# Kernel optimization log

Measured on AMD Instinct MI355X. Metric: run time of the kernel, lower is better.

Reference implementation:

```python
import jax, jax.numpy as jnp
import numpy as np

B, T, C, H = 2, 2048, 1024, 16
HS = C // H  # head_size = 64
EPS = 1e-5


def _layernorm(x, w, b):
    mu = jnp.mean(x, axis=-1, keepdims=True)
    var = jnp.mean(jnp.square(x - mu), axis=-1, keepdims=True)
    return (x - mu) * jax.lax.rsqrt(var + EPS) * w + b


def setup_inputs() -> dict:
    key = jax.random.key(0)
    ks = jax.random.split(key, 12)
    s_attn = 1.0 / np.sqrt(C)
    s_ff1 = 1.0 / np.sqrt(C)
    s_ff2 = 1.0 / np.sqrt(4 * C)
    return {
        "x": jax.random.normal(ks[0], (B, T, C), dtype=jnp.float32),
        "ln1_w": jnp.ones((C,), jnp.float32),
        "ln1_b": jnp.zeros((C,), jnp.float32),
        "Wq": jax.random.normal(ks[1], (H, C, HS), jnp.float32) * s_attn,
        "Wk": jax.random.normal(ks[2], (H, C, HS), jnp.float32) * s_attn,
        "Wv": jax.random.normal(ks[3], (H, C, HS), jnp.float32) * s_attn,
        "proj_w": jax.random.normal(ks[4], (C, C), jnp.float32) * s_attn,
        "proj_b": jnp.zeros((C,), jnp.float32),
        "ln2_w": jnp.ones((C,), jnp.float32),
        "ln2_b": jnp.zeros((C,), jnp.float32),
        "fc1_w": jax.random.normal(ks[5], (C, 4 * C), jnp.float32) * s_ff1,
        "fc1_b": jnp.zeros((4 * C,), jnp.float32),
        "fc2_w": jax.random.normal(ks[6], (4 * C, C), jnp.float32) * s_ff2,
        "fc2_b": jnp.zeros((C,), jnp.float32),
    }


def reference(x, ln1_w, ln1_b, Wq, Wk, Wv, proj_w, proj_b, ln2_w, ln2_b, fc1_w, fc1_b, fc2_w, fc2_b):
    Bx, Tx, Cx = x.shape
    # --- self-attention with pre-norm residual ---
    h = _layernorm(x, ln1_w, ln1_b)                       # [B,T,C]
    q = jnp.einsum("btc,hcd->bhtd", h, Wq)                 # [B,H,T,HS]
    k = jnp.einsum("btc,hcd->bhtd", h, Wk)
    v = jnp.einsum("btc,hcd->bhtd", h, Wv)
    # NOTE: original code applies NO 1/sqrt(d) scaling -- keep faithful.
    wei = jnp.einsum("bhtd,bhsd->bhts", q, k)              # [B,H,T,T]
    causal = jnp.tril(jnp.ones((Tx, Tx), dtype=bool))
    wei = jnp.where(causal, wei, -jnp.inf)
    wei = jax.nn.softmax(wei, axis=-1)
    attn = jnp.einsum("bhts,bhsd->bhtd", wei, v)           # [B,H,T,HS]
    attn = attn.transpose(0, 2, 1, 3).reshape(Bx, Tx, Cx)  # concat heads
    sa = attn @ proj_w + proj_b                            # output projection
    x = x + sa
    # --- FFN with pre-norm residual ---
    h2 = _layernorm(x, ln2_w, ln2_b)
    ff = jax.nn.relu(h2 @ fc1_w + fc1_b) @ fc2_w + fc2_b
    return x + ff
```

## Files before the change

### kernel.cpp

```cpp
#include <hip/hip_runtime.h>
#include <hip/hip_bf16.h>

#define Bn 2
#define Tn 2048
#define Cn 1024
#define Hn 16
#define HSn 64
#define Mn (Bn*Tn)
#define LN_EPS 1e-5f

typedef unsigned short u16;
typedef __attribute__((ext_vector_type(8))) short bf16x8;
typedef __attribute__((ext_vector_type(4))) float f32x4;

#define MFMA16(a,b,c) __builtin_amdgcn_mfma_f32_16x16x32_bf16(a, b, c, 0, 0, 0)
#define GLL16(g,l) __builtin_amdgcn_global_load_lds( \
    (const __attribute__((address_space(1))) void*)(g), \
    (__attribute__((address_space(3))) void*)(l), 16, 0, 0)

__device__ __forceinline__ u16 f2b(float f) {
    unsigned int u = __float_as_uint(f);
    unsigned int r = (u + 0x7FFFu + ((u >> 16) & 1u)) >> 16;
    return (u16)r;
}
__device__ __forceinline__ float b2f(unsigned u) {
    return __uint_as_float(u << 16);
}
__device__ __forceinline__ unsigned cvtpk(float lo, float hi) {
    unsigned r;
    asm("v_cvt_pk_bf16_f32 %0, %1, %2" : "=v"(r) : "v"(lo), "v"(hi));
    return r;
}

__device__ __forceinline__ void trans_tile(
    const float* __restrict__ in, u16* __restrict__ out,
    int R, int C, int r0, int c0c, float (*t)[68], int tid)
{
#pragma unroll
    for (int it = 0; it < 4; it++) {
        int r = it * 16 + (tid >> 4);
        *(float4*)&t[r][(tid & 15) * 4] =
            *(const float4*)(in + (size_t)(r0 + r) * C + c0c + (tid & 15) * 4);
    }
    __syncthreads();
    int c = tid >> 2, seg = tid & 3;
    union { u16 u[8]; uint4 q; } pk;
#pragma unroll
    for (int hq = 0; hq < 2; hq++) {
#pragma unroll
        for (int j = 0; j < 8; j++) pk.u[j] = f2b(t[seg * 16 + hq * 8 + j][c]);
        *(uint4*)(out + (size_t)(c0c + c) * R + r0 + seg * 16 + hq * 8) = pk.q;
    }
}

__global__ __launch_bounds__(256) void repack_all(
    const float* __restrict__ Wq, const float* __restrict__ Wk,
    const float* __restrict__ Wv, u16* __restrict__ WtQKV,
    const float* __restrict__ projw, u16* __restrict__ WtP,
    const float* __restrict__ fc1w, u16* __restrict__ Wt1,
    const float* __restrict__ fc2w, u16* __restrict__ Wt2)
{
    __shared__ float t[64][68];
    const int bid = (int)blockIdx.x, tid = threadIdx.x;
    if (bid < 768) {
        int z = bid >> 8, rem = bid & 255, h = rem >> 4, c0 = (rem & 15) * 64;
        const float* in = (z == 0 ? Wq : z == 1 ? Wk : Wv) + (size_t)h * 65536;
        u16* outb = WtQKV + (size_t)(z * 1024 + h * 64) * 1024;
        trans_tile(in, outb, 1024, 64, c0, 0, t, tid);
    } else if (bid < 1024) {
        int idx = bid - 768, bx = idx & 15, by = idx >> 4;
        trans_tile(projw, WtP, 1024, 1024, by * 64, bx * 64, t, tid);
    } else if (bid < 2048) {
        int idx = bid - 1024, bx = idx & 63, by = idx >> 6;
        trans_tile(fc1w, Wt1, 1024, 4096, by * 64, bx * 64, t, tid);
    } else {
        int idx = bid - 2048, bx = idx & 15, by = idx >> 4;
        trans_tile(fc2w, Wt2, 4096, 1024, by * 64, bx * 64, t, tid);
    }
}

__global__ __launch_bounds__(256) void ln_bf16(
    const float* __restrict__ x, const float* __restrict__ w,
    const float* __restrict__ bvec, u16* __restrict__ out)
{
    int row  = blockIdx.x * 4 + (threadIdx.x >> 6);
    int lane = threadIdx.x & 63;
    const float* xr = x + (size_t)row * Cn;
    float4 v[4];
    float s = 0.f, sq = 0.f;
#pragma unroll
    for (int i = 0; i < 4; i++) {
        v[i] = *(const float4*)(xr + lane * 4 + i * 256);
        s  += v[i].x + v[i].y + v[i].z + v[i].w;
        sq += v[i].x * v[i].x + v[i].y * v[i].y + v[i].z * v[i].z + v[i].w * v[i].w;
    }
#pragma unroll
    for (int off = 1; off < 64; off <<= 1) {
        s  += __shfl_xor(s, off);
        sq += __shfl_xor(sq, off);
    }
    float mu   = s * (1.f / Cn);
    float var  = sq * (1.f / Cn) - mu * mu;
    float rstd = rsqrtf(var + LN_EPS);
    u16* orow = out + (size_t)row * Cn;
#pragma unroll
    for (int i = 0; i < 4; i++) {
        float4 w4 = *(const float4*)(w    + lane * 4 + i * 256);
        float4 b4 = *(const float4*)(bvec + lane * 4 + i * 256);
        union { u16 u[4]; uint2 q; } pk;
        pk.u[0] = f2b((v[i].x - mu) * rstd * w4.x + b4.x);
        pk.u[1] = f2b((v[i].y - mu) * rstd * w4.y + b4.y);
        pk.u[2] = f2b((v[i].z - mu) * rstd * w4.z + b4.z);
        pk.u[3] = f2b((v[i].w - mu) * rstd * w4.w + b4.w);
        *(uint2*)(orow + lane * 4 + i * 256) = pk.q;
    }
}

__global__ __launch_bounds__(256) void ln_bf16_b(
    const u16* __restrict__ x, const float* __restrict__ w,
    const float* __restrict__ bvec, u16* __restrict__ out)
{
    int row  = blockIdx.x * 4 + (threadIdx.x >> 6);
    int lane = threadIdx.x & 63;
    const u16* xr = x + (size_t)row * Cn + lane * 16;
    float v[16];
    float s = 0.f, sq = 0.f;
#pragma unroll
    for (int i = 0; i < 2; i++) {
        uint4 q = *(const uint4*)(xr + i * 8);
        float* vv = v + i * 8;
        vv[0] = b2f(q.x & 0xffffu); vv[1] = b2f(q.x >> 16);
        vv[2] = b2f(q.y & 0xffffu); vv[3] = b2f(q.y >> 16);
        vv[4] = b2f(q.z & 0xffffu); vv[5] = b2f(q.z >> 16);
        vv[6] = b2f(q.w & 0xffffu); vv[7] = b2f(q.w >> 16);
    }
#pragma unroll
    for (int j = 0; j < 16; j++) { s += v[j]; sq += v[j] * v[j]; }
#pragma unroll
    for (int off = 1; off < 64; off <<= 1) {
        s  += __shfl_xor(s, off);
        sq += __shfl_xor(sq, off);
    }
    float mu   = s * (1.f / Cn);
    float var  = sq * (1.f / Cn) - mu * mu;
    float rstd = rsqrtf(var + LN_EPS);
    u16* orow = out + (size_t)row * Cn + lane * 16;
#pragma unroll
    for (int i = 0; i < 2; i++) {
        union { u16 u[8]; uint4 q; } pk;
#pragma unroll
        for (int j = 0; j < 8; j++) {
            int col = lane * 16 + i * 8 + j;
            pk.u[j] = f2b((v[i * 8 + j] - mu) * rstd * w[col] + bvec[col]);
        }
        *(uint4*)(orow + i * 8) = pk.q;
    }
}

template<int OBF, int BIAS, int RELU>
__global__ __launch_bounds__(512, 2) void gemm_8ph(
    const u16* __restrict__ A, const u16* __restrict__ Bt,
    const float* __restrict__ bias, void* Cout,
    int M, int N, int K, int NT)
{
    __shared__ u16 lds[65536];
    const int tid = threadIdx.x, l = tid & 63, w = tid >> 6;
    const int wm = w >> 2, wn = w & 3;
    const int g = l >> 4, c16 = l & 15;

    const int nwg = (int)gridDim.x, cpx = nwg >> 3;
    const int bid = (int)blockIdx.x;
    const int sbid = (bid & 7) * cpx + (bid >> 3);
    const int m0 = (sbid / NT) * 256, n0 = (sbid % NT) * 256;

    const int sr = tid >> 3;
    const int ss = ((tid & 7) ^ (sr & 7)) << 3;
    const u16* Asrc = A  + (size_t)(m0 + sr) * K + ss;
    const u16* Bsrc = Bt + (size_t)(n0 + sr) * K + ss;
    const int dst0 = tid * 8;

#define ST_A8(d_, h_, kt_) do {                                              \
        GLL16(Asrc + (size_t)((h_) * 128) * K + (size_t)(kt_) * 64,          \
              &lds[(d_) * 32768 + (h_) * 8192 + dst0]);                      \
        GLL16(Asrc + (size_t)((h_) * 128 + 64) * K + (size_t)(kt_) * 64,     \
              &lds[(d_) * 32768 + (h_) * 8192 + 4096 + dst0]);               \
    } while (0)
#define ST_B8(d_, h_, kt_) do {                                              \
        GLL16(Bsrc + (size_t)((h_) * 128) * K + (size_t)(kt_) * 64,          \
              &lds[(d_) * 32768 + 16384 + (h_) * 8192 + dst0]);              \
        GLL16(Bsrc + (size_t)((h_) * 128 + 64) * K + (size_t)(kt_) * 64,     \
              &lds[(d_) * 32768 + 16384 + (h_) * 8192 + 4096 + dst0]);       \
    } while (0)
#define LDA8(d_, mi_, s_) (*(const bf16x8*)&lds[(d_) * 32768 +               \
        (wm * 128 + (mi_) * 16 + c16) * 64 +                                  \
        ((((s_) * 4 + g) ^ ((wm * 128 + (mi_) * 16 + c16) & 7)) << 3)])
#define LDB8(d_, nj_, s_) (*(const bf16x8*)&lds[(d_) * 32768 + 16384 +       \
        (wn * 64 + (nj_) * 16 + c16) * 64 +                                   \
        ((((s_) * 4 + g) ^ ((wn * 64 + (nj_) * 16 + c16) & 7)) << 3)])
#define PH_HEAD() do {                                                       \
        __builtin_amdgcn_s_barrier();                                        \
        asm volatile("s_waitcnt lgkmcnt(0)" ::: "memory");                   \
        __builtin_amdgcn_sched_barrier(0);                                   \
        __builtin_amdgcn_s_setprio(1);                                       \
    } while (0)
#define PH_MFMA(NH_) do {                                                    \
        _Pragma("unroll")                                                    \
        for (int mi = 0; mi < 8; mi++) {                                     \
            acc[mi][2*(NH_)]   = MFMA16(aF[mi], bF[0], acc[mi][2*(NH_)]);    \
            acc[mi][2*(NH_)+1] = MFMA16(aF[mi], bF[1], acc[mi][2*(NH_)+1]);  \
        }                                                                    \
    } while (0)

    f32x4 acc[8][4];
#pragma unroll
    for (int i = 0; i < 8; i++)
#pragma unroll
        for (int j = 0; j < 4; j++) acc[i][j] = (f32x4){0.f, 0.f, 0.f, 0.f};

    const int nk = K >> 6;
    ST_A8(0, 0, 0); ST_A8(0, 1, 0); ST_B8(0, 0, 0); ST_B8(0, 1, 0);
    ST_A8(1, 0, 1); ST_A8(1, 1, 1);
    asm volatile("s_waitcnt vmcnt(4)" ::: "memory");
    __builtin_amdgcn_s_barrier();

    bf16x8 aF[8], bF[2];
    for (int m = 0; m < nk; m++) {
        const int d = m & 1, dn = d ^ 1;
#pragma unroll
        for (int mi = 0; mi < 8; mi++) aF[mi] = LDA8(d, mi, 0);
        bF[0] = LDB8(d, 0, 0); bF[1] = LDB8(d, 1, 0);
        if (m + 1 < nk) ST_B8(dn, 0, m + 1);
        PH_HEAD(); PH_MFMA(0);
        __builtin_amdgcn_s_setprio(0);
        __builtin_amdgcn_s_barrier();
        bF[0] = LDB8(d, 2, 0); bF[1] = LDB8(d, 3, 0);
        if (m + 1 < nk) ST_B8(dn, 1, m + 1);
        PH_HEAD(); PH_MFMA(1);
        __builtin_amdgcn_s_setprio(0);
        __builtin_amdgcn_s_barrier();
#pragma unroll
        for (int mi = 0; mi < 8; mi++) aF[mi] = LDA8(d, mi, 1);
        bF[0] = LDB8(d, 0, 1); bF[1] = LDB8(d, 1, 1);
        PH_HEAD(); PH_MFMA(0);
        __builtin_amdgcn_s_setprio(0);
        __builtin_amdgcn_s_barrier();
        bF[0] = LDB8(d, 2, 1); bF[1] = LDB8(d, 3, 1);
        if (m + 2 < nk) { ST_A8(d, 0, m + 2); ST_A8(d, 1, m + 2); }
        PH_HEAD(); PH_MFMA(1);
        __builtin_amdgcn_s_setprio(0);
        if (m + 1 < nk) {
            if (m + 2 < nk) asm volatile("s_waitcnt vmcnt(4)" ::: "memory");
            else            asm volatile("s_waitcnt vmcnt(0)" ::: "memory");
        }
        __builtin_amdgcn_s_barrier();
    }
#undef ST_A8
#undef ST_B8
#undef LDA8
#undef LDB8
#undef PH_HEAD
#undef PH_MFMA

#pragma unroll
    for (int mi = 0; mi < 8; mi++)
#pragma unroll
        for (int nj = 0; nj < 4; nj++) {
            const int coln = n0 + wn * 64 + nj * 16 + c16;
            float bv = BIAS ? bias[coln] : 0.f;
#pragma unroll
            for (int reg = 0; reg < 4; reg++) {
                int rowm = m0 + wm * 128 + mi * 16 + 4 * g + reg;
                float v = acc[mi][nj][reg] + bv;
                if (RELU) v = fmaxf(v, 0.f);
                if (OBF) ((u16*)Cout)[(size_t)rowm * N + coln] = f2b(v);
                else     ((float*)Cout)[(size_t)rowm * N + coln] = v;
            }
        }
}

__global__ __launch_bounds__(512, 1) void gemm_qkv(
    const u16* __restrict__ A, const u16* __restrict__ Bt,
    u16* __restrict__ Cout)
{
    __shared__ u16 lds[57344];
    const int tid = threadIdx.x, l = tid & 63, w = tid >> 6;
    const int wm = w >> 1, wn = w & 1;
    const int g = l >> 4, c16 = l & 15;
    const int K = 1024, N = 3072;

    const int bid = (int)blockIdx.x;
    const int sbid = (bid & 7) * 32 + (bid >> 3);
    const int m0 = (sbid >> 4) * 256, n0 = (sbid & 15) * 192;

    const int sr = tid >> 3;
    const int ss = ((tid & 7) ^ (sr & 7)) << 3;
    const u16* Asrc = A  + (size_t)(m0 + sr) * K + ss;
    const u16* Bsrc = Bt + (size_t)(n0 + sr) * K + ss;
    const int dst0 = tid * 8;

#define ST_A(d_, h_, kt_) do {                                               \
        GLL16(Asrc + (size_t)((h_) * 128) * K + (size_t)(kt_) * 64,          \
              &lds[(d_) * 16384 + (h_) * 8192 + dst0]);                      \
        GLL16(Asrc + (size_t)((h_) * 128 + 64) * K + (size_t)(kt_) * 64,     \
              &lds[(d_) * 16384 + (h_) * 8192 + 4096 + dst0]);               \
    } while (0)
#define ST_B1(d_, seg_, kt_)                                                 \
        GLL16(Bsrc + (size_t)((seg_) * 64) * K + (size_t)(kt_) * 64,         \
              &lds[32768 + (d_) * 12288 + (seg_) * 4096 + dst0])
#define LDA(d_, mi_, s_) (*(const bf16x8*)&lds[(d_) * 16384 +                \
        (wm * 64 + (mi_) * 16 + c16) * 64 +                                   \
        ((((s_) * 4 + g) ^ ((wm * 64 + (mi_) * 16 + c16) & 7)) << 3)])
#define LDB(d_, nj_, s_) (*(const bf16x8*)&lds[32768 + (d_) * 12288 +        \
        (wn * 96 + (nj_) * 16 + c16) * 64 +                                   \
        ((((s_) * 4 + g) ^ ((wn * 96 + (nj_) * 16 + c16) & 7)) << 3)])
#define PH_HEAD() do {                                                       \
        __builtin_amdgcn_s_barrier();                                        \
        asm volatile("s_waitcnt lgkmcnt(0)" ::: "memory");                   \
        __builtin_amdgcn_sched_barrier(0);                                   \
        __builtin_amdgcn_s_setprio(1);                                       \
    } while (0)
#define PH_MFMA(NH_) do {                                                    \
        _Pragma("unroll")                                                    \
        for (int mi = 0; mi < 4; mi++) {                                     \
            acc[mi][3*(NH_)]   = MFMA16(aF[mi], bF[0], acc[mi][3*(NH_)]);    \
            acc[mi][3*(NH_)+1] = MFMA16(aF[mi], bF[1], acc[mi][3*(NH_)+1]);  \
            acc[mi][3*(NH_)+2] = MFMA16(aF[mi], bF[2], acc[mi][3*(NH_)+2]);  \
        }                                                                    \
    } while (0)

    f32x4 acc[4][6];
#pragma unroll
    for (int i = 0; i < 4; i++)
#pragma unroll
        for (int j = 0; j < 6; j++) acc[i][j] = (f32x4){0.f, 0.f, 0.f, 0.f};

    const int nk = 16;
    ST_A(0, 0, 0); ST_A(0, 1, 0);
    ST_B1(0, 0, 0); ST_B1(0, 1, 0); ST_B1(0, 2, 0);
    ST_A(1, 0, 1); ST_A(1, 1, 1);
    asm volatile("s_waitcnt vmcnt(4)" ::: "memory");
    __builtin_amdgcn_s_barrier();

    bf16x8 aF[4], bF[3];
    for (int m = 0; m < nk; m++) {
        const int d = m & 1, dn = d ^ 1;
#pragma unroll
        for (int mi = 0; mi < 4; mi++) aF[mi] = LDA(d, mi, 0);
        bF[0] = LDB(d, 0, 0); bF[1] = LDB(d, 1, 0); bF[2] = LDB(d, 2, 0);
        if (m + 1 < nk) { ST_B1(dn, 0, m + 1); ST_B1(dn, 1, m + 1); }
        PH_HEAD(); PH_MFMA(0);
        __builtin_amdgcn_s_setprio(0);
        __builtin_amdgcn_s_barrier();
        bF[0] = LDB(d, 3, 0); bF[1] = LDB(d, 4, 0); bF[2] = LDB(d, 5, 0);
        if (m + 1 < nk) ST_B1(dn, 2, m + 1);
        PH_HEAD(); PH_MFMA(1);
        __builtin_amdgcn_s_setprio(0);
        __builtin_amdgcn_s_barrier();
#pragma unroll
        for (int mi = 0; mi < 4; mi++) aF[mi] = LDA(d, mi, 1);
        bF[0] = LDB(d, 0, 1); bF[1] = LDB(d, 1, 1); bF[2] = LDB(d, 2, 1);
        PH_HEAD(); PH_MFMA(0);
        __builtin_amdgcn_s_setprio(0);
        __builtin_amdgcn_s_barrier();
        bF[0] = LDB(d, 3, 1); bF[1] = LDB(d, 4, 1); bF[2] = LDB(d, 5, 1);
        if (m + 2 < nk) { ST_A(d, 0, m + 2); ST_A(d, 1, m + 2); }
        PH_HEAD(); PH_MFMA(1);
        __builtin_amdgcn_s_setprio(0);
        if (m + 1 < nk) {
            if (m + 2 < nk) asm volatile("s_waitcnt vmcnt(4)" ::: "memory");
            else            asm volatile("s_waitcnt vmcnt(0)" ::: "memory");
        }
        __builtin_amdgcn_s_barrier();
    }
#undef ST_A
#undef ST_B1
#undef LDA
#undef LDB
#undef PH_HEAD
#undef PH_MFMA

#pragma unroll
    for (int mi = 0; mi < 4; mi++)
#pragma unroll
        for (int nj = 0; nj < 6; nj++) {
            const int coln = n0 + wn * 96 + nj * 16 + c16;
#pragma unroll
            for (int reg = 0; reg < 4; reg++) {
                int rowm = m0 + wm * 64 + mi * 16 + 4 * g + reg;
                Cout[(size_t)rowm * N + coln] = f2b(acc[mi][nj][reg]);
            }
        }
}

__global__ __launch_bounds__(512, 2) void gemm_fc2(
    const u16* __restrict__ A, const u16* __restrict__ Bt,
    u16* __restrict__ part)
{
    __shared__ u16 lds[65536];
    const int tid = threadIdx.x, l = tid & 63, w = tid >> 6;
    const int wm = w >> 2, wn = w & 3;
    const int g = l >> 4, c16 = l & 15;

    const int bid = (int)blockIdx.x;
    const int sbid = (bid & 7) * 32 + (bid >> 3);
    const int chunk = sbid >> 6, t = sbid & 63;
    const int m0 = (t >> 2) * 256, n0 = (t & 3) * 256;
    const int kB = chunk << 10;

    const int sr = tid >> 3;
    const int ss = ((tid & 7) ^ (sr & 7)) << 3;
    const u16* Asrc = A  + (size_t)(m0 + sr) * 4096 + kB + ss;
    const u16* Bsrc = Bt + (size_t)(n0 + sr) * 4096 + kB + ss;
    const int dst0 = tid * 8;

#define ST_A8(d_, h_, kt_) do {                                              \
        GLL16(Asrc + (size_t)((h_) * 128) * 4096 + (size_t)(kt_) * 64,       \
              &lds[(d_) * 32768 + (h_) * 8192 + dst0]);                      \
        GLL16(Asrc + (size_t)((h_) * 128 + 64) * 4096 + (size_t)(kt_) * 64,  \
              &lds[(d_) * 32768 + (h_) * 8192 + 4096 + dst0]);               \
    } while (0)
#define ST_B8(d_, h_, kt_) do {                                              \
        GLL16(Bsrc + (size_t)((h_) * 128) * 4096 + (size_t)(kt_) * 64,       \
              &lds[(d_) * 32768 + 16384 + (h_) * 8192 + dst0]);              \
        GLL16(Bsrc + (size_t)((h_) * 128 + 64) * 4096 + (size_t)(kt_) * 64,  \
              &lds[(d_) * 32768 + 16384 + (h_) * 8192 + 4096 + dst0]);       \
    } while (0)
#define LDA8(d_, mi_, s_) (*(const bf16x8*)&lds[(d_) * 32768 +               \
        (wm * 128 + (mi_) * 16 + c16) * 64 +                                  \
        ((((s_) * 4 + g) ^ ((wm * 128 + (mi_) * 16 + c16) & 7)) << 3)])
#define LDB8(d_, nj_, s_) (*(const bf16x8*)&lds[(d_) * 32768 + 16384 +       \
        (wn * 64 + (nj_) * 16 + c16) * 64 +                                   \
        ((((s_) * 4 + g) ^ ((wn * 64 + (nj_) * 16 + c16) & 7)) << 3)])
#define PH_HEAD() do {                                                       \
        __builtin_amdgcn_s_barrier();                                        \
        asm volatile("s_waitcnt lgkmcnt(0)" ::: "memory");                   \
        __builtin_amdgcn_sched_barrier(0);                                   \
        __builtin_amdgcn_s_setprio(1);                                       \
    } while (0)
#define PH_MFMA(NH_) do {                                                    \
        _Pragma("unroll")                                                    \
        for (int mi = 0; mi < 8; mi++) {                                     \
            acc[mi][2*(NH_)]   = MFMA16(aF[mi], bF[0], acc[mi][2*(NH_)]);    \
            acc[mi][2*(NH_)+1] = MFMA16(aF[mi], bF[1], acc[mi][2*(NH_)+1]);  \
        }                                                                    \
    } while (0)

    f32x4 acc[8][4];
#pragma unroll
    for (int i = 0; i < 8; i++)
#pragma unroll
        for (int j = 0; j < 4; j++) acc[i][j] = (f32x4){0.f, 0.f, 0.f, 0.f};

    const int nk = 16;
    ST_A8(0, 0, 0); ST_A8(0, 1, 0); ST_B8(0, 0, 0); ST_B8(0, 1, 0);
    ST_A8(1, 0, 1); ST_A8(1, 1, 1);
    asm volatile("s_waitcnt vmcnt(4)" ::: "memory");
    __builtin_amdgcn_s_barrier();

    bf16x8 aF[8], bF[2];
    for (int m = 0; m < nk; m++) {
        const int d = m & 1, dn = d ^ 1;
#pragma unroll
        for (int mi = 0; mi < 8; mi++) aF[mi] = LDA8(d, mi, 0);
        bF[0] = LDB8(d, 0, 0); bF[1] = LDB8(d, 1, 0);
        if (m + 1 < nk) ST_B8(dn, 0, m + 1);
        PH_HEAD(); PH_MFMA(0);
        __builtin_amdgcn_s_setprio(0);
        __builtin_amdgcn_s_barrier();
        bF[0] = LDB8(d, 2, 0); bF[1] = LDB8(d, 3, 0);
        if (m + 1 < nk) ST_B8(dn, 1, m + 1);
        PH_HEAD(); PH_MFMA(1);
        __builtin_amdgcn_s_setprio(0);
        __builtin_amdgcn_s_barrier();
#pragma unroll
        for (int mi = 0; mi < 8; mi++) aF[mi] = LDA8(d, mi, 1);
        bF[0] = LDB8(d, 0, 1); bF[1] = LDB8(d, 1, 1);
        PH_HEAD(); PH_MFMA(0);
        __builtin_amdgcn_s_setprio(0);
        __builtin_amdgcn_s_barrier();
        bF[0] = LDB8(d, 2, 1); bF[1] = LDB8(d, 3, 1);
        if (m + 2 < nk) { ST_A8(d, 0, m + 2); ST_A8(d, 1, m + 2); }
        PH_HEAD(); PH_MFMA(1);
        __builtin_amdgcn_s_setprio(0);
        if (m + 1 < nk) {
            if (m + 2 < nk) asm volatile("s_waitcnt vmcnt(4)" ::: "memory");
            else            asm volatile("s_waitcnt vmcnt(0)" ::: "memory");
        }
        __builtin_amdgcn_s_barrier();
    }
#undef ST_A8
#undef ST_B8
#undef LDA8
#undef LDB8
#undef PH_HEAD
#undef PH_MFMA

    u16* pp = part + (size_t)chunk * 4194304;
#pragma unroll
    for (int mi = 0; mi < 8; mi++)
#pragma unroll
        for (int nj = 0; nj < 4; nj++) {
            const int coln = n0 + wn * 64 + nj * 16 + c16;
#pragma unroll
            for (int reg = 0; reg < 4; reg++) {
                int rowm = m0 + wm * 128 + mi * 16 + 4 * g + reg;
                pp[(size_t)rowm * 1024 + coln] = f2b(acc[mi][nj][reg]);
            }
        }
}

__global__ __launch_bounds__(256) void splitk_reduce(
    const u16* __restrict__ part, const u16* __restrict__ x1,
    const float* __restrict__ bias, float* __restrict__ out)
{
    size_t i = ((size_t)blockIdx.x * 256 + threadIdx.x) * 4;
    int col = (int)(i & 1023);
    float4 bv = *(const float4*)(bias + col);
    uint2 xv = *(const uint2*)(x1 + i);
    float s0 = b2f(xv.x & 0xffffu) + bv.x;
    float s1 = b2f(xv.x >> 16)     + bv.y;
    float s2 = b2f(xv.y & 0xffffu) + bv.z;
    float s3 = b2f(xv.y >> 16)     + bv.w;
#pragma unroll
    for (int c = 0; c < 4; c++) {
        uint2 p = *(const uint2*)(part + (size_t)c * 4194304 + i);
        s0 += b2f(p.x & 0xffffu);
        s1 += b2f(p.x >> 16);
        s2 += b2f(p.y & 0xffffu);
        s3 += b2f(p.y >> 16);
    }
    float4 r; r.x = s0; r.y = s1; r.z = s2; r.w = s3;
    *(float4*)(out + i) = r;
}

template<int OBF, int BIAS, int RES, int RELU>
__global__ __launch_bounds__(256) void gemm_n64(
    const u16* __restrict__ A, const u16* __restrict__ Bt,
    const float* __restrict__ bias, const float* res,
    void* Cout, int M, int N, int K)
{
    __shared__ u16 As[2][8192];
    __shared__ u16 Bs[2][4096];
    const int tid = threadIdx.x;
    const int l = tid & 63, w = tid >> 6;
    const int wr = w >> 1, wc = w & 1;
    const int g = l >> 4, c16 = l & 15;
    const int m0 = blockIdx.y * 128, n0 = blockIdx.x * 64;

    const u16* a_src[4];
    int a_dst[4];
#pragma unroll
    for (int i = 0; i < 4; i++) {
        int G = tid + 256 * i, r = G >> 3, sl = G & 7;
        a_src[i] = A + (size_t)(m0 + r) * K + ((sl ^ (r & 7)) << 3);
        a_dst[i] = G * 8;
    }
    const u16* b_src[2];
    int b_dst[2];
#pragma unroll
    for (int i = 0; i < 2; i++) {
        int G = tid + 256 * i, r = G >> 3, sl = G & 7;
        b_src[i] = Bt + (size_t)(n0 + r) * K + ((sl ^ (r & 7)) << 3);
        b_dst[i] = G * 8;
    }

    f32x4 acc[4][2];
#pragma unroll
    for (int i = 0; i < 4; i++)
#pragma unroll
        for (int j = 0; j < 2; j++) acc[i][j] = (f32x4){0.f, 0.f, 0.f, 0.f};

#define STAGE_N64(nb, k0) do {                                   \
        GLL16(a_src[0] + (k0), &As[nb][a_dst[0]]);               \
        GLL16(a_src[1] + (k0), &As[nb][a_dst[1]]);               \
        GLL16(a_src[2] + (k0), &As[nb][a_dst[2]]);               \
        GLL16(a_src[3] + (k0), &As[nb][a_dst[3]]);               \
        GLL16(b_src[0] + (k0), &Bs[nb][b_dst[0]]);               \
        GLL16(b_src[1] + (k0), &Bs[nb][b_dst[1]]);               \
    } while (0)

    STAGE_N64(0, 0);
    __syncthreads();

    int cur = 0;
    for (int k0 = 0; k0 < K; k0 += 64) {
        if (k0 + 64 < K) STAGE_N64(cur ^ 1, k0 + 64);
        const u16* AsC = As[cur];
        const u16* BsC = Bs[cur];
        bf16x8 af[4][2], bfr[2][2];
#pragma unroll
        for (int fi = 0; fi < 4; fi++) {
            int r = wr * 64 + fi * 16 + c16;
            af[fi][0] = *(const bf16x8*)&AsC[r * 64 + (((g    ) ^ (r & 7)) << 3)];
            af[fi][1] = *(const bf16x8*)&AsC[r * 64 + (((4 + g) ^ (r & 7)) << 3)];
        }
#pragma unroll
        for (int fj = 0; fj < 2; fj++) {
            int r = wc * 32 + fj * 16 + c16;
            bfr[fj][0] = *(const bf16x8*)&BsC[r * 64 + (((g    ) ^ (r & 7)) << 3)];
            bfr[fj][1] = *(const bf16x8*)&BsC[r * 64 + (((4 + g) ^ (r & 7)) << 3)];
        }
#pragma unroll
        for (int fi = 0; fi < 4; fi++)
#pragma unroll
            for (int fj = 0; fj < 2; fj++) {
                acc[fi][fj] = MFMA16(af[fi][0], bfr[fj][0], acc[fi][fj]);
                acc[fi][fj] = MFMA16(af[fi][1], bfr[fj][1], acc[fi][fj]);
            }
        __syncthreads();
        cur ^= 1;
    }
#undef STAGE_N64

#pragma unroll
    for (int fi = 0; fi < 4; fi++)
#pragma unroll
        for (int fj = 0; fj < 2; fj++) {
            int coln = n0 + wc * 32 + fj * 16 + c16;
            float bv = BIAS ? bias[coln] : 0.f;
#pragma unroll
            for (int reg = 0; reg < 4; reg++) {
                int rowm = m0 + wr * 64 + fi * 16 + 4 * g + reg;
                float v = acc[fi][fj][reg] + bv;
                if (RES) v += res[(size_t)rowm * N + coln];
                if (RELU) v = fmaxf(v, 0.f);
                if (OBF) ((u16*)Cout)[(size_t)rowm * N + coln] = f2b(v);
                else     ((float*)Cout)[(size_t)rowm * N + coln] = v;
            }
        }
}

__global__ __launch_bounds__(256) void v_transpose(
    const u16* __restrict__ qkv, u16* __restrict__ vT)
{
    int t0 = blockIdx.x * 64, h = blockIdx.y, b = blockIdx.z;
    __shared__ u16 t[64][72];
    int tid = threadIdx.x;
#pragma unroll
    for (int it = 0; it < 2; it++) {
        int r = it * 32 + (tid >> 3);
        int cs = (tid & 7) * 8;
        *(uint4*)&t[r][cs] =
            *(const uint4*)(qkv + (size_t)(b * 2048 + t0 + r) * 3072 + 2048 + h * 64 + cs);
    }
    __syncthreads();
    int d = tid >> 2, seg = tid & 3;
    union { u16 u[8]; uint4 q; } pk;
#pragma unroll
    for (int hq = 0; hq < 2; hq++) {
#pragma unroll
        for (int j = 0; j < 8; j++) pk.u[j] = t[seg * 16 + hq * 8 + j][d];
        *(uint4*)(vT + (size_t)((b * 16 + h) * 64 + d) * 2048 + t0 + seg * 16 + hq * 8) = pk.q;
    }
}

__global__ __launch_bounds__(512) void attn_mfma(
    const u16* __restrict__ qkv, const u16* __restrict__ vT,
    u16* __restrict__ outb)
{
    __shared__ u16 smem[24576];
    u16* KsB = smem;
    u16* VsB = smem + 8192;
    u16* PsB = smem + 16384;
    const int tid = threadIdx.x, l = tid & 63, w = tid >> 6;
    const int g = l >> 4, c16 = l & 15;
    const int qg = w & 3, kg = w >> 2;
    const int kg32 = kg * 32, kg64 = kg * 64;
    const int bh = blockIdx.y, b = bh >> 4, h = bh & 15;
    const int bx = (int)blockIdx.x;
    const int qt = (bh < 16) ? (15 - bx) : bx;
    const int r0 = qt * 128;
    const int wq0 = r0 + qg * 32;

    bf16x8 qf[2][2];
#pragma unroll
    for (int grp = 0; grp < 2; grp++) {
        const u16* qrow = qkv + (size_t)(b * 2048 + wq0 + grp * 16 + c16) * 3072 + h * 64;
        qf[grp][0] = *(const bf16x8*)(qrow + g * 8);
        qf[grp][1] = *(const bf16x8*)(qrow + 32 + g * 8);
    }

    const int kr = tid >> 3, ks = (tid & 7) ^ (kr & 7);
    const u16* kgp = qkv + (size_t)(b * 2048) * 3072 + 1024 + h * 64;
    const u16* vgp = vT + (size_t)((b * 16 + h) * 64) * 2048;

    float lrow[2] = {0.f, 0.f};
    f32x4 oacc[2][4];
#pragma unroll
    for (int grp = 0; grp < 2; grp++)
#pragma unroll
        for (int i = 0; i < 4; i++) oacc[grp][i] = (f32x4){0.f, 0.f, 0.f, 0.f};

    const int prow0 = (qg * 32 + c16) * 128;
    const int swz   = (c16 & 7) << 4;

#define STAGE_KV(nb, s0) do {                                                  \
        GLL16(kgp + (size_t)((s0) + kr) * 3072 + ks * 8, &KsB[(nb)*4096 + tid*8]); \
        GLL16(vgp + (size_t)kr * 2048 + (s0) + ks * 8, &VsB[(nb)*4096 + tid*8]);   \
    } while (0)

    STAGE_KV(0, 0);
    asm volatile("s_waitcnt vmcnt(0)" ::: "memory");
    __builtin_amdgcn_sched_barrier(0);
    __builtin_amdgcn_s_barrier();

    const int nt = 2 * qt + 2;
    int cur = 0;
    for (int kt = 0; kt < nt; kt++) {
        if (kt + 1 < nt) STAGE_KV(cur ^ 1, (kt + 1) * 64);
        if (kt > 0) {
            if (kt + 1 < nt) asm volatile("s_waitcnt vmcnt(2)" ::: "memory");
            else             asm volatile("s_waitcnt vmcnt(0)" ::: "memory");
            __builtin_amdgcn_sched_barrier(0);
            __builtin_amdgcn_s_barrier();
        }
        const u16* KsC = &KsB[cur * 4096];
        const u16* VsC = &VsB[cur * 4096];
        const int s0 = kt * 64;

        bf16x8 kf0[2], kf1[2];
#pragma unroll
        for (int fj = 0; fj < 2; fj++) {
            int r = kg32 + fj * 16 + c16;
            kf0[fj] = *(const bf16x8*)&KsC[r * 64 + ((g       ^ (r & 7)) << 3)];
            kf1[fj] = *(const bf16x8*)&KsC[r * 64 + (((4 + g) ^ (r & 7)) << 3)];
        }
#pragma unroll
        for (int grp = 0; grp < 2; grp++) {
            f32x4 sc[2];
            sc[0] = (f32x4){0.f, 0.f, 0.f, 0.f};
            sc[1] = (f32x4){0.f, 0.f, 0.f, 0.f};
#pragma unroll
            for (int fj = 0; fj < 2; fj++) {
                sc[fj] = MFMA16(kf0[fj], qf[grp][0], sc[fj]);
                sc[fj] = MFMA16(kf1[fj], qf[grp][1], sc[fj]);
            }
            const int qgl = wq0 + grp * 16 + c16;
            if (s0 + kg32 + 31 > wq0 + grp * 16) {
#pragma unroll
                for (int fj = 0; fj < 2; fj++)
#pragma unroll
                    for (int reg = 0; reg < 4; reg++)
                        if (s0 + kg32 + fj * 16 + 4 * g + reg > qgl)
                            sc[fj][reg] = -1e30f;
            }
#pragma unroll
            for (int fj = 0; fj < 2; fj++) {
                float p0 = __expf(sc[fj][0]);
                float p1 = __expf(sc[fj][1]);
                float p2 = __expf(sc[fj][2]);
                float p3 = __expf(sc[fj][3]);
                lrow[grp] += (p0 + p1) + (p2 + p3);
                uint2 pk;
                pk.x = cvtpk(p0, p1);
                pk.y = cvtpk(p2, p3);
                *(uint2*)((char*)PsB + prow0 + grp * 2048 +
                          ((kg64 + fj * 32 + 8 * g) ^ swz)) = pk;
            }
        }
        bf16x8 pa0 = *(const bf16x8*)((const char*)PsB + prow0 +
                                      ((kg64 + 16 * g) ^ swz));
        bf16x8 pa1 = *(const bf16x8*)((const char*)PsB + prow0 + 2048 +
                                      ((kg64 + 16 * g) ^ swz));
#pragma unroll
        for (int fd = 0; fd < 4; fd++) {
            int r = fd * 16 + c16;
            bf16x8 vf = *(const bf16x8*)&VsC[r * 64 + (((4 * kg + g) ^ (r & 7)) << 3)];
            oacc[0][fd] = MFMA16(pa0, vf, oacc[0][fd]);
            oacc[1][fd] = MFMA16(pa1, vf, oacc[1][fd]);
        }
        __builtin_amdgcn_s_barrier();
        cur ^= 1;
    }
#undef STAGE_KV

#pragma unroll
    for (int grp = 0; grp < 2; grp++) {
        lrow[grp] += __shfl_xor(lrow[grp], 16);
        lrow[grp] += __shfl_xor(lrow[grp], 32);
    }

    __syncthreads();
    float* scr = (float*)smem;
    const int sbase = qg * 2304 + l * 36;
    if (kg == 1) {
#pragma unroll
        for (int grp = 0; grp < 2; grp++) {
#pragma unroll
            for (int fd = 0; fd < 4; fd++)
                *(f32x4*)&scr[sbase + grp * 16 + fd * 4] = oacc[grp][fd];
            scr[sbase + 32 + grp] = lrow[grp];
        }
    }
    __syncthreads();
    if (kg == 0) {
#pragma unroll
        for (int grp = 0; grp < 2; grp++) {
#pragma unroll
            for (int fd = 0; fd < 4; fd++)
                oacc[grp][fd] += *(const f32x4*)&scr[sbase + grp * 16 + fd * 4];
            float lr = lrow[grp] + scr[sbase + 32 + grp];
#pragma unroll
            for (int reg = 0; reg < 4; reg++) {
                float ls = __shfl(lr, 4 * g + reg);
                float inv = 1.0f / ls;
                int t = wq0 + grp * 16 + 4 * g + reg;
                u16* op = outb + (size_t)(b * 2048 + t) * 1024 + h * 64;
#pragma unroll
                for (int fd = 0; fd < 4; fd++)
                    op[fd * 16 + c16] = f2b(oacc[grp][fd][reg] * inv);
            }
        }
    }
}

extern "C" void kernel_launch(void* const* d_in, const int* in_sizes, int n_in,
                              void* d_out, int out_size, void* d_ws, size_t ws_size,
                              hipStream_t stream) {
    const float* x     = (const float*)d_in[0];
    const float* ln1w  = (const float*)d_in[1];
    const float* ln1b  = (const float*)d_in[2];
    const float* Wq    = (const float*)d_in[3];
    const float* Wk    = (const float*)d_in[4];
    const float* Wv    = (const float*)d_in[5];
    const float* projw = (const float*)d_in[6];
    const float* projb = (const float*)d_in[7];
    const float* ln2w  = (const float*)d_in[8];
    const float* ln2b  = (const float*)d_in[9];
    const float* fc1w  = (const float*)d_in[10];
    const float* fc1b  = (const float*)d_in[11];
    const float* fc2w  = (const float*)d_in[12];
    const float* fc2b  = (const float*)d_in[13];
    float* out = (float*)d_out;

    u16* h_bf    = (u16*)d_ws;
    u16* qkv_bf  = h_bf    + 4194304;
    u16* vTb     = qkv_bf  + 12582912;
    u16* attn_bf = vTb     + 4194304;
    u16* ff1_bf  = attn_bf + 4194304;
    u16* WtQKV   = ff1_bf  + 16777216;
    u16* WtP     = WtQKV   + 3145728;
    u16* Wt1     = WtP     + 1048576;
    u16* Wt2     = Wt1     + 4194304;
    u16* x1_bf   = Wt2     + 4194304;
    u16* fc2p = (u16*)d_ws;

    repack_all<<<dim3(3072), 256, 0, stream>>>(
        Wq, Wk, Wv, WtQKV, projw, WtP, fc1w, Wt1, fc2w, Wt2);

    ln_bf16<<<1024, 256, 0, stream>>>(x, ln1w, ln1b, h_bf);
    gemm_qkv<<<dim3(256), 512, 0, stream>>>(h_bf, WtQKV, qkv_bf);
    v_transpose<<<dim3(32, 16, 2), 256, 0, stream>>>(qkv_bf, vTb);
    attn_mfma<<<dim3(16, 32), 512, 0, stream>>>(qkv_bf, vTb, attn_bf);
    gemm_n64<1, 1, 1, 0><<<dim3(16, 32), 256, 0, stream>>>(
        attn_bf, WtP, projb, x, x1_bf, Mn, 1024, 1024);
    ln_bf16_b<<<1024, 256, 0, stream>>>(x1_bf, ln2w, ln2b, h_bf);
    gemm_8ph<1, 1, 1><<<dim3(256), 512, 0, stream>>>(
        h_bf, Wt1, fc1b, ff1_bf, Mn, 4096, 1024, 16);
    gemm_fc2<<<dim3(256), 512, 0, stream>>>(ff1_bf, Wt2, fc2p);
    splitk_reduce<<<dim3(4096), 256, 0, stream>>>(fc2p, x1_bf, fc2b, out);
}
```

Baseline: 199.3 us.

## Replace 256x256 fc1 GEMM with 128x256 tile, BK=32 double-buffered kernel

Replaces the generic 8-phase 256x256-tile GEMM for fc1 with a specialized kernel using 128x256 tiles, K-step 32, a simple double-buffered LDS pipeline, and 4 blocks per CU. The grid doubles to 512 blocks, with smaller LDS use and fewer accumulators, to raise occupancy and improve load balance across CUs. In exchange, each tile reuses its operands less, and the shallower K step means more barriers per unit of work.

```diff
diff --git a/kernel.cpp b/kernel.cpp
--- a/kernel.cpp
+++ b/kernel.cpp
@@ -157,123 +157,89 @@
     }
 }
 
-template<int OBF, int BIAS, int RELU>
-__global__ __launch_bounds__(512, 2) void gemm_8ph(
+__global__ __launch_bounds__(512, 4) void gemm_fc1(
     const u16* __restrict__ A, const u16* __restrict__ Bt,
-    const float* __restrict__ bias, void* Cout,
-    int M, int N, int K, int NT)
-{
-    __shared__ u16 lds[65536];
+    const float* __restrict__ bias, u16* __restrict__ Cout)
+{
+    __shared__ u16 lds[24576];
     const int tid = threadIdx.x, l = tid & 63, w = tid >> 6;
     const int wm = w >> 2, wn = w & 3;
     const int g = l >> 4, c16 = l & 15;
-
-    const int nwg = (int)gridDim.x, cpx = nwg >> 3;
+    const int K = 1024, N = 4096;
+
     const int bid = (int)blockIdx.x;
-    const int sbid = (bid & 7) * cpx + (bid >> 3);
-    const int m0 = (sbid / NT) * 256, n0 = (sbid % NT) * 256;
-
-    const int sr = tid >> 3;
-    const int ss = ((tid & 7) ^ (sr & 7)) << 3;
-    const u16* Asrc = A  + (size_t)(m0 + sr) * K + ss;
-    const u16* Bsrc = Bt + (size_t)(n0 + sr) * K + ss;
-    const int dst0 = tid * 8;
-
-#define ST_A8(d_, h_, kt_) do {                                              \
-        GLL16(Asrc + (size_t)((h_) * 128) * K + (size_t)(kt_) * 64,          \
-              &lds[(d_) * 32768 + (h_) * 8192 + dst0]);                      \
-        GLL16(Asrc + (size_t)((h_) * 128 + 64) * K + (size_t)(kt_) * 64,     \
-              &lds[(d_) * 32768 + (h_) * 8192 + 4096 + dst0]);               \
-    } while (0)
-#define ST_B8(d_, h_, kt_) do {                                              \
-        GLL16(Bsrc + (size_t)((h_) * 128) * K + (size_t)(kt_) * 64,          \
-              &lds[(d_) * 32768 + 16384 + (h_) * 8192 + dst0]);              \
-        GLL16(Bsrc + (size_t)((h_) * 128 + 64) * K + (size_t)(kt_) * 64,     \
-              &lds[(d_) * 32768 + 16384 + (h_) * 8192 + 4096 + dst0]);       \
-    } while (0)
-#define LDA8(d_, mi_, s_) (*(const bf16x8*)&lds[(d_) * 32768 +               \
-        (wm * 128 + (mi_) * 16 + c16) * 64 +                                  \
-        ((((s_) * 4 + g) ^ ((wm * 128 + (mi_) * 16 + c16) & 7)) << 3)])
-#define LDB8(d_, nj_, s_) (*(const bf16x8*)&lds[(d_) * 32768 + 16384 +       \
-        (wn * 64 + (nj_) * 16 + c16) * 64 +                                   \
-        ((((s_) * 4 + g) ^ ((wn * 64 + (nj_) * 16 + c16) & 7)) << 3)])
-#define PH_HEAD() do {                                                       \
-        __builtin_amdgcn_s_barrier();                                        \
-        asm volatile("s_waitcnt lgkmcnt(0)" ::: "memory");                   \
-        __builtin_amdgcn_sched_barrier(0);                                   \
-        __builtin_amdgcn_s_setprio(1);                                       \
-    } while (0)
-#define PH_MFMA(NH_) do {                                                    \
-        _Pragma("unroll")                                                    \
-        for (int mi = 0; mi < 8; mi++) {                                     \
-            acc[mi][2*(NH_)]   = MFMA16(aF[mi], bF[0], acc[mi][2*(NH_)]);    \
-            acc[mi][2*(NH_)+1] = MFMA16(aF[mi], bF[1], acc[mi][2*(NH_)+1]);  \
-        }                                                                    \
-    } while (0)
-
-    f32x4 acc[8][4];
-#pragma unroll
-    for (int i = 0; i < 8; i++)
+    const int sbid = (bid & 7) * 64 + (bid >> 3);
+    const int m0 = (sbid >> 4) * 128, n0 = (sbid & 15) * 256;
+
+    const int ar = tid >> 2, as = ((tid & 3) ^ (ar & 3)) << 3;
+    const u16* a0 = A + (size_t)(m0 + ar) * K + as;
+    const int br0 = tid >> 2,        bs0 = ((tid & 3) ^ (br0 & 3)) << 3;
+    const int br1 = (tid + 512) >> 2, bs1 = (((tid + 512) & 3) ^ (br1 & 3)) << 3;
+    const u16* b0 = Bt + (size_t)(n0 + br0) * K + bs0;
+    const u16* b1 = Bt + (size_t)(n0 + br1) * K + bs1;
+
+#define STG_F1(dd, kt) do {                                              \
+        GLL16(a0 + (size_t)(kt) * 32, &lds[(dd) * 4096 + tid * 8]);      \
+        GLL16(b0 + (size_t)(kt) * 32, &lds[8192 + (dd) * 8192 + tid * 8]); \
+        GLL16(b1 + (size_t)(kt) * 32, &lds[8192 + (dd) * 8192 + 4096 + tid * 8]); \
+    } while (0)
+#define LDA_F1(dd, mi) (*(const bf16x8*)&lds[(dd) * 4096 +               \
+        (wm * 64 + (mi) * 16 + c16) * 32 +                                \
+        ((g ^ ((wm * 64 + (mi) * 16 + c16) & 3)) << 3)])
+#define LDB_F1(dd, nj) (*(const bf16x8*)&lds[8192 + (dd) * 8192 +        \
+        (wn * 64 + (nj) * 16 + c16) * 32 +                                \
+        ((g ^ ((wn * 64 + (nj) * 16 + c16) & 3)) << 3)])
+
+    f32x4 acc[4][4];
+#pragma unroll
+    for (int i = 0; i < 4; i++)
 #pragma unroll
         for (int j = 0; j < 4; j++) acc[i][j] = (f32x4){0.f, 0.f, 0.f, 0.f};
 
-    const int nk = K >> 6;
-    ST_A8(0, 0, 0); ST_A8(0, 1, 0); ST_B8(0, 0, 0); ST_B8(0, 1, 0);
-    ST_A8(1, 0, 1); ST_A8(1, 1, 1);
-    asm volatile("s_waitcnt vmcnt(4)" ::: "memory");
+    const int nk = 32;
+    STG_F1(0, 0);
+    asm volatile("s_waitcnt vmcnt(0)" ::: "memory");
+    __builtin_amdgcn_sched_barrier(0);
     __builtin_amdgcn_s_barrier();
 
-    bf16x8 aF[8], bF[2];
     for (int m = 0; m < nk; m++) {
         const int d = m & 1, dn = d ^ 1;
-#pragma unroll
-        for (int mi = 0; mi < 8; mi++) aF[mi] = LDA8(d, mi, 0);
-        bF[0] = LDB8(d, 0, 0); bF[1] = LDB8(d, 1, 0);
-        if (m + 1 < nk) ST_B8(dn, 0, m + 1);
-        PH_HEAD(); PH_MFMA(0);
+        if (m + 1 < nk) STG_F1(dn, m + 1);
+        if (m > 0) {
+            if (m + 1 < nk) asm volatile("s_waitcnt vmcnt(3)" ::: "memory");
+            else            asm volatile("s_waitcnt vmcnt(0)" ::: "memory");
+            __builtin_amdgcn_sched_barrier(0);
+            __builtin_amdgcn_s_barrier();
+        }
+        bf16x8 aF[4], bF[4];
+#pragma unroll
+        for (int mi = 0; mi < 4; mi++) aF[mi] = LDA_F1(d, mi);
+#pragma unroll
+        for (int nj = 0; nj < 4; nj++) bF[nj] = LDB_F1(d, nj);
+        __builtin_amdgcn_s_setprio(1);
+#pragma unroll
+        for (int mi = 0; mi < 4; mi++)
+#pragma unroll
+            for (int nj = 0; nj < 4; nj++)
+                acc[mi][nj] = MFMA16(aF[mi], bF[nj], acc[mi][nj]);
         __builtin_amdgcn_s_setprio(0);
         __builtin_amdgcn_s_barrier();
-        bF[0] = LDB8(d, 2, 0); bF[1] = LDB8(d, 3, 0);
-        if (m + 1 < nk) ST_B8(dn, 1, m + 1);
-        PH_HEAD(); PH_MFMA(1);
-        __builtin_amdgcn_s_setprio(0);
-        __builtin_amdgcn_s_barrier();
-#pragma unroll
-        for (int mi = 0; mi < 8; mi++) aF[mi] = LDA8(d, mi, 1);
-        bF[0] = LDB8(d, 0, 1); bF[1] = LDB8(d, 1, 1);
-        PH_HEAD(); PH_MFMA(0);
-        __builtin_amdgcn_s_setprio(0);
-        __builtin_amdgcn_s_barrier();
-        bF[0] = LDB8(d, 2, 1); bF[1] = LDB8(d, 3, 1);
-        if (m + 2 < nk) { ST_A8(d, 0, m + 2); ST_A8(d, 1, m + 2); }
-        PH_HEAD(); PH_MFMA(1);
-        __builtin_amdgcn_s_setprio(0);
-        if (m + 1 < nk) {
-            if (m + 2 < nk) asm volatile("s_waitcnt vmcnt(4)" ::: "memory");
-            else            asm volatile("s_waitcnt vmcnt(0)" ::: "memory");
-        }
-        __builtin_amdgcn_s_barrier();
-    }
-#undef ST_A8
-#undef ST_B8
-#undef LDA8
-#undef LDB8
-#undef PH_HEAD
-#undef PH_MFMA
-
-#pragma unroll
-    for (int mi = 0; mi < 8; mi++)
+    }
+#undef STG_F1
+#undef LDA_F1
+#undef LDB_F1
+
+#pragma unroll
+    for (int mi = 0; mi < 4; mi++)
 #pragma unroll
         for (int nj = 0; nj < 4; nj++) {
             const int coln = n0 + wn * 64 + nj * 16 + c16;
-            float bv = BIAS ? bias[coln] : 0.f;
+            float bv = bias[coln];
 #pragma unroll
             for (int reg = 0; reg < 4; reg++) {
-                int rowm = m0 + wm * 128 + mi * 16 + 4 * g + reg;
-                float v = acc[mi][nj][reg] + bv;
-                if (RELU) v = fmaxf(v, 0.f);
-                if (OBF) ((u16*)Cout)[(size_t)rowm * N + coln] = f2b(v);
-                else     ((float*)Cout)[(size_t)rowm * N + coln] = v;
+                int rowm = m0 + wm * 64 + mi * 16 + 4 * g + reg;
+                float v = fmaxf(acc[mi][nj][reg] + bv, 0.f);
+                Cout[(size_t)rowm * N + coln] = f2b(v);
             }
         }
 }
@@ -855,8 +821,7 @@
     gemm_n64<1, 1, 1, 0><<<dim3(16, 32), 256, 0, stream>>>(
         attn_bf, WtP, projb, x, x1_bf, Mn, 1024, 1024);
     ln_bf16_b<<<1024, 256, 0, stream>>>(x1_bf, ln2w, ln2b, h_bf);
-    gemm_8ph<1, 1, 1><<<dim3(256), 512, 0, stream>>>(
-        h_bf, Wt1, fc1b, ff1_bf, Mn, 4096, 1024, 16);
+    gemm_fc1<<<dim3(512), 512, 0, stream>>>(h_bf, Wt1, fc1b, ff1_bf);
     gemm_fc2<<<dim3(256), 512, 0, stream>>>(ff1_bf, Wt2, fc2p);
     splitk_reduce<<<dim3(4096), 256, 0, stream>>>(fc2p, x1_bf, fc2b, out);
 }
```

After: 202.3 us. No clear change (+1.5%).
